# Performance work log

Hardware: AMD Instinct MI355X
Metric: run time of the kernel (lower is better)

Reference implementation:

```python
import jax, jax.numpy as jnp
import numpy as np

EPS = 1e-5


def _bn_relu(h, gamma, beta):
    # BatchNorm1d in training mode: stats over all but the last (channel) dim
    m = h.reshape(-1, h.shape[-1])
    mu = jnp.mean(m, axis=0)
    var = jnp.var(m, axis=0)
    return jax.nn.relu((h - mu) * jax.lax.rsqrt(var + EPS) * gamma + beta)


def setup_inputs() -> dict:
    key = jax.random.key(0)
    ks = jax.random.split(key, 16)
    B, N, D, OUT = 64, 64, 64, 128
    T = 2 * D          # object_tuple_size = 128
    HG, HF = 256, 128  # hidden_dim_g, hidden_dim_f

    def lin(k, i, o):
        return (jax.random.normal(k, (i, o), jnp.float32) / np.sqrt(i).astype(np.float32),
                jnp.zeros((o,), jnp.float32))

    inp = {"x": jax.random.normal(ks[0], (B, N, D), jnp.float32)}
    # G: depth-3 Linear-BN-ReLU, dims T -> HG -> HG -> T
    for i, (a, b) in enumerate([(T, HG), (HG, HG), (HG, T)]):
        W, bb = lin(ks[1 + i], a, b)
        inp[f"gW{i}"] = W
        inp[f"gb{i}"] = bb
        inp[f"gg{i}"] = jnp.ones((b,), jnp.float32)
        inp[f"gB{i}"] = jnp.zeros((b,), jnp.float32)
    # F: depth-2 Linear-BN-ReLU, dims T -> HF -> T, then Linear(T, OUT)
    for i, (a, b) in enumerate([(T, HF), (HF, T)]):
        W, bb = lin(ks[5 + i], a, b)
        inp[f"fW{i}"] = W
        inp[f"fb{i}"] = bb
        inp[f"fg{i}"] = jnp.ones((b,), jnp.float32)
        inp[f"fB{i}"] = jnp.zeros((b,), jnp.float32)
    inp["foW"], inp["fob"] = lin(ks[8], T, OUT)
    return inp


def reference(x, gW0, gb0, gg0, gB0, gW1, gb1, gg1, gB1, gW2, gb2, gg2, gB2,
              fW0, fb0, fg0, fB0, fW1, fb1, fg1, fB1, foW, fob):
    B, N, D = x.shape
    # GroupObjectsIntoPairs: all ordered pairs -> (B, N*N, 2D)
    xi = jnp.broadcast_to(x[:, :, None, :], (B, N, N, D))
    xj = jnp.broadcast_to(x[:, None, :, :], (B, N, N, D))
    h = jnp.concatenate([xi, xj], axis=-1).reshape(B, N * N, 2 * D)
    # G: per-pair MLP
    for W, b, g, be in ((gW0, gb0, gg0, gB0), (gW1, gb1, gg1, gB1), (gW2, gb2, gg2, gB2)):
        h = _bn_relu(h @ W + b, g, be)
    # sum over pair dimension (no layer norm)
    s = h.sum(axis=1)  # (B, 2D)
    # F: MLP + final linear
    for W, b, g, be in ((fW0, fb0, fg0, fB0), (fW1, fb1, fg1, fB1)):
        s = _bn_relu(s @ W + b, g, be)
    return s @ foW + fob  # (B, OUT)
```

## Files before the change

### kernel.cpp

```cpp
#include <hip/hip_runtime.h>


typedef _Float16 half8 __attribute__((ext_vector_type(8)));
typedef _Float16 half4_t __attribute__((ext_vector_type(4)));
typedef float float4_t __attribute__((ext_vector_type(4)));

static constexpr float kEps = 1e-5f;
static constexpr float kM = 262144.f;

static constexpr size_t OFF_U   = 0;
static constexpr size_t OFF_V   = OFF_U  + (size_t)4096*256*4;
static constexpr size_t OFF_UP  = OFF_V  + (size_t)4096*256*4;
static constexpr size_t OFF_VP  = OFF_UP + (size_t)4096*256*2;
static constexpr size_t OFF_W1T = OFF_VP + (size_t)4096*256*2;
static constexpr size_t OFF_W2T = OFF_W1T + (size_t)256*256*2;
static constexpr size_t OFF_Z1  = OFF_W2T + (size_t)128*256*2;
static constexpr size_t OFF_ST0 = OFF_Z1 + (size_t)262144*256*2;
static constexpr size_t OFF_C0S = OFF_ST0 + (size_t)64*4*256*4;
static constexpr size_t OFF_C0T = OFF_C0S + 1024;
static constexpr size_t OFF_C1S = OFF_C0T + 1024;
static constexpr size_t OFF_C1T = OFF_C1S + 1024;
static constexpr size_t OFF_C2S = OFF_C1T + 1024;
static constexpr size_t OFF_C2T = OFF_C2S + 512;
static constexpr size_t OFF_ST1 = OFF_C2T + 512;
static constexpr size_t OFF_ST2 = OFF_ST1 + (size_t)32*512*4;
static constexpr size_t OFF_SB  = OFF_ST2 + (size_t)32*256*4;
static constexpr size_t OFF_FST0 = OFF_SB + (size_t)64*128*4;
static constexpr size_t OFF_FST1 = OFF_FST0 + 1024;
static constexpr size_t ZERO_BYTES = (size_t)32*512*4 + (size_t)32*256*4
                                   + (size_t)64*128*4 + 2048;
static constexpr size_t OFF_FZ0  = OFF_FST1 + 1024;
static constexpr size_t OFF_FZ1  = OFF_FZ0 + (size_t)64*128*4;
static constexpr size_t OFF_CF0S = OFF_FZ1 + (size_t)64*128*4;
static constexpr size_t OFF_CF0T = OFF_CF0S + 512;
static constexpr size_t OFF_CF1S = OFF_CF0T + 512;
static constexpr size_t OFF_CF1T = OFF_CF1S + 512;
static constexpr size_t OFF_C1H  = OFF_CF1T + 512;
static constexpr size_t OFF_Z2   = OFF_C1H + 1024;
static constexpr size_t WS_REQUIRED = OFF_Z2 + (size_t)262144*128*2;

static __device__ inline half8 relu8(half8 s) {
#pragma unroll
  for (int e = 0; e < 8; ++e) s[e] = s[e] > (_Float16)0 ? s[e] : (_Float16)0;
  return s;
}

__global__ __launch_bounds__(256) void k_wt(const float* __restrict__ gW1,
                                            const float* __restrict__ gW2,
                                            _Float16* __restrict__ W1T,
                                            _Float16* __restrict__ W2T) {
  int idx = blockIdx.x * 256 + threadIdx.x;
  if (idx < 65536) {
    int n = idx >> 8, k = idx & 255;
    W1T[idx] = (_Float16)gW1[k * 256 + n];
  } else if (idx < 98304) {
    int j = idx - 65536;
    int n = j >> 8, k = j & 255;
    W2T[j] = (_Float16)gW2[k * 128 + n];
  }
}

__global__ __launch_bounds__(256) void k_prep(const float* __restrict__ x,
                                              const float* __restrict__ gW0,
                                              float* __restrict__ U,
                                              float* __restrict__ V) {
  __shared__ __align__(16) float sX[32 * 64];
  int t = threadIdx.x;
  int p0 = blockIdx.x * 32;
  int by = blockIdx.y;
  int hsel = by >> 1;
  int cbase = (by & 1) * 128;
#pragma unroll
  for (int it = 0; it < 2; ++it) {
    int f4 = (it * 256 + t) * 4;
    *(float4_t*)(sX + f4) = *(const float4_t*)(x + (size_t)p0 * 64 + f4);
  }
  __syncthreads();
  int r = t >> 3, cg = (t & 7) * 16;
  const float* Wb = gW0 + (size_t)(hsel * 64) * 256 + cbase + cg;
  float acc[16];
#pragma unroll
  for (int j = 0; j < 16; ++j) acc[j] = 0.f;
  for (int k = 0; k < 64; ++k) {
    float xv = sX[r * 64 + k];
    const float4_t* wr = (const float4_t*)(Wb + (size_t)k * 256);
    float4_t w0 = wr[0], w1 = wr[1], w2 = wr[2], w3 = wr[3];
#pragma unroll
    for (int j = 0; j < 4; ++j) {
      acc[j]      += xv * w0[j];
      acc[4 + j]  += xv * w1[j];
      acc[8 + j]  += xv * w2[j];
      acc[12 + j] += xv * w3[j];
    }
  }
  float* outp = (hsel ? V : U) + (size_t)(p0 + r) * 256 + cbase + cg;
#pragma unroll
  for (int q = 0; q < 4; ++q) {
    float4_t o = {acc[q * 4], acc[q * 4 + 1], acc[q * 4 + 2], acc[q * 4 + 3]};
    *(float4_t*)(outp + q * 4) = o;
  }
}

__global__ __launch_bounds__(256) void k_stats0(const float* __restrict__ U,
                                                const float* __restrict__ V,
                                                float* __restrict__ st0) {
  int b = blockIdx.x, c = threadIdx.x;
  float su = 0, su2 = 0, sv = 0, sv2 = 0;
  for (int i = 0; i < 64; ++i) {
    float u = U[(size_t)(b * 64 + i) * 256 + c];
    float v = V[(size_t)(b * 64 + i) * 256 + c];
    su += u; su2 += u * u; sv += v; sv2 += v * v;
  }
  st0[(b * 4 + 0) * 256 + c] = su;
  st0[(b * 4 + 1) * 256 + c] = su2;
  st0[(b * 4 + 2) * 256 + c] = sv;
  st0[(b * 4 + 3) * 256 + c] = sv2;
}

__global__ __launch_bounds__(256) void k_bn0(const float* __restrict__ st0,
                                             const float* __restrict__ gb0,
                                             const float* __restrict__ gg0,
                                             const float* __restrict__ gB0,
                                             float* __restrict__ c0s,
                                             float* __restrict__ c0t) {
  int c = threadIdx.x;
  float su = 0, su2 = 0, sv = 0, sv2 = 0, cross = 0;
  for (int b = 0; b < 64; ++b) {
    float a  = st0[(b * 4 + 0) * 256 + c];
    float a2 = st0[(b * 4 + 1) * 256 + c];
    float v  = st0[(b * 4 + 2) * 256 + c];
    float v2 = st0[(b * 4 + 3) * 256 + c];
    su += a; su2 += a2; sv += v; sv2 += v2; cross += a * v;
  }
  float b0 = gb0[c];
  float sumz  = 64.f * (su + sv) + kM * b0;
  float sumzz = 64.f * (su2 + sv2) + 2.f * cross + 2.f * b0 * 64.f * (su + sv) + kM * b0 * b0;
  float mu = sumz / kM;
  float var = sumzz / kM - mu * mu;
  float sc = gg0[c] * rsqrtf(var + kEps);
  c0s[c] = sc;
  c0t[c] = gB0[c] + sc * (b0 - mu);
}

__global__ __launch_bounds__(256) void k_uv(const float* __restrict__ U,
                                            const float* __restrict__ V,
                                            const float* __restrict__ c0s,
                                            const float* __restrict__ c0t,
                                            _Float16* __restrict__ Up,
                                            _Float16* __restrict__ Vp) {
  int idx = blockIdx.x * 256 + threadIdx.x;
  int e4 = idx * 4;
  int c4 = e4 & 255;
  float4_t u = *(const float4_t*)(U + e4);
  float4_t v = *(const float4_t*)(V + e4);
  float4_t s = *(const float4_t*)(c0s + c4);
  float4_t tt = *(const float4_t*)(c0t + c4);
  half4_t hu, hv;
#pragma unroll
  for (int e = 0; e < 4; ++e) {
    hu[e] = (_Float16)(u[e] * s[e] + tt[e]);
    hv[e] = (_Float16)(v[e] * s[e]);
  }
  *(half4_t*)(Up + e4) = hu;
  *(half4_t*)(Vp + e4) = hv;
}

__global__ __launch_bounds__(256) void k_gemm1(const _Float16* __restrict__ Up,
                                               const _Float16* __restrict__ Vp,
                                               const _Float16* __restrict__ W1T,
                                               const float* __restrict__ gb1,
                                               _Float16* __restrict__ Z1,
                                               float* __restrict__ stats1) {
  __shared__ __align__(16) _Float16 sU[2 * 264];
  __shared__ __align__(16) _Float16 sV[64 * 264];
  __shared__ __align__(16) _Float16 sW[128 * 72];
  const int t = threadIdx.x;
  const int bx = blockIdx.x;
  const int n0 = blockIdx.y * 128;
  const int b = bx >> 5;
  const int i0 = (bx & 31) * 2;
  const long R0 = (long)bx * 128;

  if (t < 64) {
    int row = t >> 5, k8 = (t & 31) * 8;
    *(half8*)(sU + row * 264 + k8) =
        *(const half8*)(Up + (size_t)(b * 64 + i0 + row) * 256 + k8);
  }
#pragma unroll
  for (int it = 0; it < 8; ++it) {
    int flat = it * 256 + t;
    int row = flat >> 5, k8 = (flat & 31) * 8;
    *(half8*)(sV + row * 264 + k8) =
        *(const half8*)(Vp + (size_t)(b * 64 + row) * 256 + k8);
  }

  const int wid = t >> 6, L = t & 63;
  const int wrow = wid >> 1, wcol = wid & 1;
  const int quad = L >> 4, l15 = L & 15;

  float4_t acc[4][4];
#pragma unroll
  for (int mt = 0; mt < 4; ++mt)
#pragma unroll
    for (int nt = 0; nt < 4; ++nt) acc[mt][nt] = (float4_t){0.f, 0.f, 0.f, 0.f};

  for (int kc = 0; kc < 4; ++kc) {
    __syncthreads();
#pragma unroll
    for (int it = 0; it < 4; ++it) {
      int flat = it * 256 + t;
      int n = flat >> 3, k8 = (flat & 7) * 8;
      *(half8*)(sW + n * 72 + k8) =
          *(const half8*)(W1T + (size_t)(n0 + n) * 256 + kc * 64 + k8);
    }
    __syncthreads();
#pragma unroll
    for (int ks = 0; ks < 2; ++ks) {
      const int kk = ks * 32 + quad * 8;
      const int kg = kc * 64 + kk;
      const half8 u = *(const half8*)(sU + wrow * 264 + kg);
      half8 afr[4];
#pragma unroll
      for (int mt = 0; mt < 4; ++mt) {
        half8 v = *(const half8*)(sV + (mt * 16 + l15) * 264 + kg);
        afr[mt] = relu8(u + v);
      }
      half8 bfr[4];
#pragma unroll
      for (int nt = 0; nt < 4; ++nt)
        bfr[nt] = *(const half8*)(sW + (wcol * 64 + nt * 16 + l15) * 72 + kk);
#pragma unroll
      for (int mt = 0; mt < 4; ++mt)
#pragma unroll
        for (int nt = 0; nt < 4; ++nt)
          acc[mt][nt] = __builtin_amdgcn_mfma_f32_16x16x32_f16(afr[mt], bfr[nt],
                                                               acc[mt][nt], 0, 0, 0);
    }
  }

  const int rep = bx & 31;
#pragma unroll
  for (int nt = 0; nt < 4; ++nt) {
    const int col = n0 + wcol * 64 + nt * 16 + l15;
    const float b1c = gb1[col];
    float sz = 0.f, szz = 0.f;
#pragma unroll
    for (int mt = 0; mt < 4; ++mt) {
      const size_t rowb = (size_t)(R0 + wrow * 64 + mt * 16 + quad * 4);
#pragma unroll
      for (int r = 0; r < 4; ++r) {
        float z = acc[mt][nt][r] + b1c;
        Z1[(rowb + r) * 256 + col] = (_Float16)z;
        sz += z;
        szz += z * z;
      }
    }
    sz += __shfl_xor(sz, 16, 64);
    sz += __shfl_xor(sz, 32, 64);
    szz += __shfl_xor(szz, 16, 64);
    szz += __shfl_xor(szz, 32, 64);
    if (quad == 0) {
      atomicAdd(stats1 + rep * 512 + col, sz);
      atomicAdd(stats1 + rep * 512 + 256 + col, szz);
    }
  }
}

__global__ __launch_bounds__(256) void k_bn1(const float* __restrict__ stats1,
                                             const float* __restrict__ gg1,
                                             const float* __restrict__ gB1,
                                             float* __restrict__ c1s,
                                             float* __restrict__ c1t,
                                             _Float16* __restrict__ c1h) {
  int c = threadIdx.x;
  float S = 0.f, S2 = 0.f;
  for (int rp = 0; rp < 32; ++rp) {
    S += stats1[rp * 512 + c];
    S2 += stats1[rp * 512 + 256 + c];
  }
  float mu = S / kM;
  float var = S2 / kM - mu * mu;
  float sc = gg1[c] * rsqrtf(var + kEps);
  float sh = gB1[c] - sc * mu;
  c1s[c] = sc;
  c1t[c] = sh;
  c1h[c] = (_Float16)sc;
  c1h[256 + c] = (_Float16)sh;
}

__global__ __launch_bounds__(256) void k_gemm2(const _Float16* __restrict__ Z1,
                                               const _Float16* __restrict__ W2T,
                                               const _Float16* __restrict__ c1h,
                                               const float* __restrict__ gb2,
                                               _Float16* __restrict__ Z2,
                                               float* __restrict__ stats2) {
  __shared__ __align__(16) _Float16 sA[128 * 72];
  __shared__ __align__(16) _Float16 sW[128 * 72];
  __shared__ __align__(16) _Float16 sSh[256];
  __shared__ __align__(16) _Float16 sTh[256];
  const int t = threadIdx.x;
  const int bx = blockIdx.x;
  const long R0 = (long)bx * 128;
  sSh[t] = c1h[t];
  sTh[t] = c1h[256 + t];

  const int wid = t >> 6, L = t & 63;
  const int wrow = wid >> 1, wcol = wid & 1;
  const int quad = L >> 4, l15 = L & 15;

  float4_t acc[4][4];
#pragma unroll
  for (int mt = 0; mt < 4; ++mt)
#pragma unroll
    for (int nt = 0; nt < 4; ++nt) acc[mt][nt] = (float4_t){0.f, 0.f, 0.f, 0.f};

  for (int kc = 0; kc < 4; ++kc) {
    __syncthreads();
#pragma unroll
    for (int it = 0; it < 4; ++it) {
      int flat = it * 256 + t;
      int row = flat >> 3, k8 = (flat & 7) * 8;
      int kg = kc * 64 + k8;
      half8 hv = *(const half8*)(Z1 + ((size_t)R0 + row) * 256 + kg);
      half8 hs = *(const half8*)(sSh + kg);
      half8 ht = *(const half8*)(sTh + kg);
      half8 ov = hv * hs + ht;
      ov = relu8(ov);
      *(half8*)(sA + row * 72 + k8) = ov;
    }
#pragma unroll
    for (int it = 0; it < 4; ++it) {
      int flat = it * 256 + t;
      int n = flat >> 3, k8 = (flat & 7) * 8;
      *(half8*)(sW + n * 72 + k8) =
          *(const half8*)(W2T + (size_t)n * 256 + kc * 64 + k8);
    }
    __syncthreads();
#pragma unroll
    for (int ks = 0; ks < 2; ++ks) {
      const int kk = ks * 32 + quad * 8;
      half8 afr[4];
#pragma unroll
      for (int mt = 0; mt < 4; ++mt)
        afr[mt] = *(const half8*)(sA + (wrow * 64 + mt * 16 + l15) * 72 + kk);
      half8 bfr[4];
#pragma unroll
      for (int nt = 0; nt < 4; ++nt)
        bfr[nt] = *(const half8*)(sW + (wcol * 64 + nt * 16 + l15) * 72 + kk);
#pragma unroll
      for (int mt = 0; mt < 4; ++mt)
#pragma unroll
        for (int nt = 0; nt < 4; ++nt)
          acc[mt][nt] = __builtin_amdgcn_mfma_f32_16x16x32_f16(afr[mt], bfr[nt],
                                                               acc[mt][nt], 0, 0, 0);
    }
  }

  const int rep = bx & 31;
#pragma unroll
  for (int nt = 0; nt < 4; ++nt) {
    const int col = wcol * 64 + nt * 16 + l15;
    const float b2c = gb2[col];
    float sz = 0.f, szz = 0.f;
#pragma unroll
    for (int mt = 0; mt < 4; ++mt) {
      const size_t rowb = (size_t)(R0 + wrow * 64 + mt * 16 + quad * 4);
#pragma unroll
      for (int r = 0; r < 4; ++r) {
        float z = acc[mt][nt][r] + b2c;
        Z2[(rowb + r) * 128 + col] = (_Float16)z;
        sz += z;
        szz += z * z;
      }
    }
    sz += __shfl_xor(sz, 16, 64);
    sz += __shfl_xor(sz, 32, 64);
    szz += __shfl_xor(szz, 16, 64);
    szz += __shfl_xor(szz, 32, 64);
    if (quad == 0) {
      atomicAdd(stats2 + rep * 256 + col, sz);
      atomicAdd(stats2 + rep * 256 + 128 + col, szz);
    }
  }
}

template <int FINAL>
__global__ __launch_bounds__(256) void k_gemm23(const _Float16* __restrict__ Z1,
                                                const _Float16* __restrict__ W2T,
                                                const float* __restrict__ c1s,
                                                const float* __restrict__ c1t,
                                                const float* __restrict__ gb2,
                                                const float* __restrict__ c2s,
                                                const float* __restrict__ c2t,
                                                float* __restrict__ stats2,
                                                float* __restrict__ sbuf) {
  __shared__ __align__(16) _Float16 sA[128 * 72];
  __shared__ __align__(16) _Float16 sW[128 * 72];
  __shared__ __align__(16) float sS[256];
  __shared__ __align__(16) float sT[256];
  const int t = threadIdx.x;
  const int bx = blockIdx.x;
  const long R0 = (long)bx * 128;
  sS[t] = c1s[t];
  sT[t] = c1t[t];

  const int wid = t >> 6, L = t & 63;
  const int wrow = wid >> 1, wcol = wid & 1;
  const int quad = L >> 4, l15 = L & 15;

  float4_t acc[4][4];
#pragma unroll
  for (int mt = 0; mt < 4; ++mt)
#pragma unroll
    for (int nt = 0; nt < 4; ++nt) acc[mt][nt] = (float4_t){0.f, 0.f, 0.f, 0.f};

  for (int kc = 0; kc < 4; ++kc) {
    __syncthreads();
#pragma unroll
    for (int it = 0; it < 4; ++it) {
      int flat = it * 256 + t;
      int row = flat >> 3, k8 = (flat & 7) * 8;
      int kg = kc * 64 + k8;
      half8 hv = *(const half8*)(Z1 + ((size_t)R0 + row) * 256 + kg);
      float4_t s0 = *(const float4_t*)(sS + kg);
      float4_t s1 = *(const float4_t*)(sS + kg + 4);
      float4_t t0 = *(const float4_t*)(sT + kg);
      float4_t t1 = *(const float4_t*)(sT + kg + 4);
      half8 ov;
#pragma unroll
      for (int e = 0; e < 4; ++e) {
        ov[e]     = (_Float16)fmaxf(s0[e] * (float)hv[e] + t0[e], 0.f);
        ov[4 + e] = (_Float16)fmaxf(s1[e] * (float)hv[4 + e] + t1[e], 0.f);
      }
      *(half8*)(sA + row * 72 + k8) = ov;
    }
#pragma unroll
    for (int it = 0; it < 4; ++it) {
      int flat = it * 256 + t;
      int n = flat >> 3, k8 = (flat & 7) * 8;
      *(half8*)(sW + n * 72 + k8) =
          *(const half8*)(W2T + (size_t)n * 256 + kc * 64 + k8);
    }
    __syncthreads();
#pragma unroll
    for (int ks = 0; ks < 2; ++ks) {
      const int kk = ks * 32 + quad * 8;
      half8 afr[4];
#pragma unroll
      for (int mt = 0; mt < 4; ++mt)
        afr[mt] = *(const half8*)(sA + (wrow * 64 + mt * 16 + l15) * 72 + kk);
      half8 bfr[4];
#pragma unroll
      for (int nt = 0; nt < 4; ++nt)
        bfr[nt] = *(const half8*)(sW + (wcol * 64 + nt * 16 + l15) * 72 + kk);
#pragma unroll
      for (int mt = 0; mt < 4; ++mt)
#pragma unroll
        for (int nt = 0; nt < 4; ++nt)
          acc[mt][nt] = __builtin_amdgcn_mfma_f32_16x16x32_f16(afr[mt], bfr[nt],
                                                               acc[mt][nt], 0, 0, 0);
    }
  }

  const int rep = bx & 31;
#pragma unroll
  for (int nt = 0; nt < 4; ++nt) {
    const int col = wcol * 64 + nt * 16 + l15;
    const float b2c = gb2[col];
    if (FINAL) {
      const float s2 = c2s[col], t2 = c2t[col];
      float ps = 0.f;
#pragma unroll
      for (int mt = 0; mt < 4; ++mt)
#pragma unroll
        for (int r = 0; r < 4; ++r)
          ps += fmaxf(s2 * (acc[mt][nt][r] + b2c) + t2, 0.f);
      ps += __shfl_xor(ps, 16, 64);
      ps += __shfl_xor(ps, 32, 64);
      if (quad == 0) atomicAdd(sbuf + (bx >> 5) * 128 + col, ps);
    } else {
      float sz = 0.f, szz = 0.f;
#pragma unroll
      for (int mt = 0; mt < 4; ++mt)
#pragma unroll
        for (int r = 0; r < 4; ++r) {
          float z = acc[mt][nt][r] + b2c;
          sz += z;
          szz += z * z;
        }
      sz += __shfl_xor(sz, 16, 64);
      sz += __shfl_xor(sz, 32, 64);
      szz += __shfl_xor(szz, 16, 64);
      szz += __shfl_xor(szz, 32, 64);
      if (quad == 0) {
        atomicAdd(stats2 + rep * 256 + col, sz);
        atomicAdd(stats2 + rep * 256 + 128 + col, szz);
      }
    }
  }
}

__global__ __launch_bounds__(128) void k_bn2(const float* __restrict__ stats2,
                                             const float* __restrict__ gg2,
                                             const float* __restrict__ gB2,
                                             float* __restrict__ c2s,
                                             float* __restrict__ c2t) {
  int c = threadIdx.x;
  float S = 0.f, S2 = 0.f;
  for (int rp = 0; rp < 32; ++rp) {
    S += stats2[rp * 256 + c];
    S2 += stats2[rp * 256 + 128 + c];
  }
  float mu = S / kM;
  float var = S2 / kM - mu * mu;
  float sc = gg2[c] * rsqrtf(var + kEps);
  c2s[c] = sc;
  c2t[c] = gB2[c] - sc * mu;
}

__global__ __launch_bounds__(256) void k_red(const _Float16* __restrict__ Z2,
                                             const float* __restrict__ c2s,
                                             const float* __restrict__ c2t,
                                             float* __restrict__ sbuf) {
  __shared__ float sR[256 * 8];
  const int t = threadIdx.x;
  const int bx = blockIdx.x;
  const int b = bx >> 5;
  const long row0 = (long)bx * 128;
  const int rr = t >> 4;
  const int c8 = (t & 15) * 8;

  float4_t s0 = *(const float4_t*)(c2s + c8);
  float4_t s1 = *(const float4_t*)(c2s + c8 + 4);
  float4_t t0 = *(const float4_t*)(c2t + c8);
  float4_t t1 = *(const float4_t*)(c2t + c8 + 4);

  float acc[8];
#pragma unroll
  for (int e = 0; e < 8; ++e) acc[e] = 0.f;
#pragma unroll
  for (int it = 0; it < 8; ++it) {
    long row = row0 + it * 16 + rr;
    half8 h = *(const half8*)(Z2 + row * 128 + c8);
#pragma unroll
    for (int e = 0; e < 4; ++e) {
      acc[e]     += fmaxf(s0[e] * (float)h[e] + t0[e], 0.f);
      acc[4 + e] += fmaxf(s1[e] * (float)h[4 + e] + t1[e], 0.f);
    }
  }
#pragma unroll
  for (int e = 0; e < 8; ++e) sR[t * 8 + e] = acc[e];
  __syncthreads();
  if (t < 128) {
    int g = t >> 3, e = t & 7;
    float S = 0.f;
#pragma unroll
    for (int rr2 = 0; rr2 < 16; ++rr2) S += sR[rr2 * 128 + t];
    (void)g; (void)e;
    atomicAdd(sbuf + b * 128 + t, S);
  }
}

template <bool APPLY_BN, bool STATS>
__global__ __launch_bounds__(256) void k_fg(const float* __restrict__ in,
                                            const float* __restrict__ cs,
                                            const float* __restrict__ ct,
                                            const float* __restrict__ W,
                                            const float* __restrict__ bias,
                                            float* __restrict__ zout,
                                            float* __restrict__ stats) {
  __shared__ __align__(16) float sIn[8 * 128];
  __shared__ __align__(16) float sZ[8 * 128];
  const int t = threadIdx.x;
  const int r0 = blockIdx.x * 8;
  {
    int flat = t * 4;
    int col = flat & 127;
    float4_t v = *(const float4_t*)(in + (size_t)r0 * 128 + flat);
    if (APPLY_BN) {
      float4_t s = *(const float4_t*)(cs + col);
      float4_t sh = *(const float4_t*)(ct + col);
#pragma unroll
      for (int e = 0; e < 4; ++e) v[e] = fmaxf(s[e] * v[e] + sh[e], 0.f);
    }
    *(float4_t*)(sIn + flat) = v;
  }
  __syncthreads();

  const int r = t >> 5;
  const int c4 = (t & 31) * 4;
  float4_t acc = *(const float4_t*)(bias + c4);
  for (int k = 0; k < 128; ++k) {
    float xv = sIn[r * 128 + k];
    float4_t w = *(const float4_t*)(W + (size_t)k * 128 + c4);
#pragma unroll
    for (int e = 0; e < 4; ++e) acc[e] += xv * w[e];
  }
  *(float4_t*)(zout + (size_t)(r0 + r) * 128 + c4) = acc;

  if (STATS) {
    *(float4_t*)(sZ + r * 128 + c4) = acc;
    __syncthreads();
    if (t < 128) {
      float S = 0.f, S2 = 0.f;
#pragma unroll
      for (int rr = 0; rr < 8; ++rr) {
        float z = sZ[rr * 128 + t];
        S += z;
        S2 += z * z;
      }
      atomicAdd(stats + t, S);
      atomicAdd(stats + 128 + t, S2);
    }
  }
}

__global__ __launch_bounds__(128) void k_fbn(const float* __restrict__ stats,
                                             const float* __restrict__ g,
                                             const float* __restrict__ B,
                                             float* __restrict__ cs,
                                             float* __restrict__ ct) {
  int c = threadIdx.x;
  float S = stats[c], S2 = stats[128 + c];
  float mu = S / 64.f;
  float var = S2 / 64.f - mu * mu;
  float sc = g[c] * rsqrtf(var + kEps);
  cs[c] = sc;
  ct[c] = B[c] - sc * mu;
}

extern "C" void kernel_launch(void* const* d_in, const int* in_sizes, int n_in,
                              void* d_out, int out_size, void* d_ws, size_t ws_size,
                              hipStream_t stream) {
  (void)in_sizes; (void)n_in; (void)out_size;
  const float* x   = (const float*)d_in[0];
  const float* gW0 = (const float*)d_in[1];
  const float* gb0 = (const float*)d_in[2];
  const float* gg0 = (const float*)d_in[3];
  const float* gB0 = (const float*)d_in[4];
  const float* gW1 = (const float*)d_in[5];
  const float* gb1 = (const float*)d_in[6];
  const float* gg1 = (const float*)d_in[7];
  const float* gB1 = (const float*)d_in[8];
  const float* gW2 = (const float*)d_in[9];
  const float* gb2 = (const float*)d_in[10];
  const float* gg2 = (const float*)d_in[11];
  const float* gB2 = (const float*)d_in[12];
  const float* fW0 = (const float*)d_in[13];
  const float* fb0 = (const float*)d_in[14];
  const float* fg0 = (const float*)d_in[15];
  const float* fB0 = (const float*)d_in[16];
  const float* fW1 = (const float*)d_in[17];
  const float* fb1 = (const float*)d_in[18];
  const float* fg1 = (const float*)d_in[19];
  const float* fB1 = (const float*)d_in[20];
  const float* foW = (const float*)d_in[21];
  const float* fob = (const float*)d_in[22];
  float* out = (float*)d_out;

  char* ws = (char*)d_ws;
  float*    U    = (float*)(ws + OFF_U);
  float*    V    = (float*)(ws + OFF_V);
  _Float16* Up   = (_Float16*)(ws + OFF_UP);
  _Float16* Vp   = (_Float16*)(ws + OFF_VP);
  _Float16* W1T  = (_Float16*)(ws + OFF_W1T);
  _Float16* W2T  = (_Float16*)(ws + OFF_W2T);
  _Float16* Z1   = (_Float16*)(ws + OFF_Z1);
  float*    st0  = (float*)(ws + OFF_ST0);
  float*    c0s  = (float*)(ws + OFF_C0S);
  float*    c0t  = (float*)(ws + OFF_C0T);
  float*    c1s  = (float*)(ws + OFF_C1S);
  float*    c1t  = (float*)(ws + OFF_C1T);
  float*    c2s  = (float*)(ws + OFF_C2S);
  float*    c2t  = (float*)(ws + OFF_C2T);
  float*    st1  = (float*)(ws + OFF_ST1);
  float*    st2  = (float*)(ws + OFF_ST2);
  float*    sbuf = (float*)(ws + OFF_SB);
  float*    fst0 = (float*)(ws + OFF_FST0);
  float*    fst1 = (float*)(ws + OFF_FST1);
  float*    fz0  = (float*)(ws + OFF_FZ0);
  float*    fz1  = (float*)(ws + OFF_FZ1);
  float*    cf0s = (float*)(ws + OFF_CF0S);
  float*    cf0t = (float*)(ws + OFF_CF0T);
  float*    cf1s = (float*)(ws + OFF_CF1S);
  float*    cf1t = (float*)(ws + OFF_CF1T);
  _Float16* c1h  = (_Float16*)(ws + OFF_C1H);
  _Float16* Z2   = (_Float16*)(ws + OFF_Z2);

  hipMemsetAsync(ws + OFF_ST1, 0, ZERO_BYTES, stream);

  k_wt<<<384, 256, 0, stream>>>(gW1, gW2, W1T, W2T);
  k_prep<<<dim3(128, 4), 256, 0, stream>>>(x, gW0, U, V);
  k_stats0<<<64, 256, 0, stream>>>(U, V, st0);
  k_bn0<<<1, 256, 0, stream>>>(st0, gb0, gg0, gB0, c0s, c0t);
  k_uv<<<1024, 256, 0, stream>>>(U, V, c0s, c0t, Up, Vp);
  k_gemm1<<<dim3(2048, 2), 256, 0, stream>>>(Up, Vp, W1T, gb1, Z1, st1);
  k_bn1<<<1, 256, 0, stream>>>(st1, gg1, gB1, c1s, c1t, c1h);

  if (ws_size >= WS_REQUIRED) {
    k_gemm2<<<2048, 256, 0, stream>>>(Z1, W2T, c1h, gb2, Z2, st2);
    k_bn2<<<1, 128, 0, stream>>>(st2, gg2, gB2, c2s, c2t);
    k_red<<<2048, 256, 0, stream>>>(Z2, c2s, c2t, sbuf);
  } else {
    k_gemm23<0><<<2048, 256, 0, stream>>>(Z1, W2T, c1s, c1t, gb2, c2s, c2t, st2, sbuf);
    k_bn2<<<1, 128, 0, stream>>>(st2, gg2, gB2, c2s, c2t);
    k_gemm23<1><<<2048, 256, 0, stream>>>(Z1, W2T, c1s, c1t, gb2, c2s, c2t, st2, sbuf);
  }

  k_fg<false, true><<<8, 256, 0, stream>>>(sbuf, nullptr, nullptr, fW0, fb0, fz0, fst0);
  k_fbn<<<1, 128, 0, stream>>>(fst0, fg0, fB0, cf0s, cf0t);
  k_fg<true, true><<<8, 256, 0, stream>>>(fz0, cf0s, cf0t, fW1, fb1, fz1, fst1);
  k_fbn<<<1, 128, 0, stream>>>(fst1, fg1, fB1, cf1s, cf1t);
  k_fg<true, false><<<8, 256, 0, stream>>>(fz1, cf1s, cf1t, foW, fob, out, nullptr);
}
```

Baseline: 322.1 us.

## Stage GEMM outputs through LDS for coalesced stores and shrink gemm1 shared memory

In k_gemm1 and k_gemm2 the MFMA accumulator results are now written into a padded LDS tile and then copied to global memory as 16-byte row-contiguous chunks. This replaces scattered 2-byte per-lane stores of Z1/Z2. k_gemm1 also loads U and V per K-chunk instead of preloading the full 256-wide rows, and reuses that buffer for output staging. This cuts LDS use from about 53KB to 35KB, which may raise occupancy. The cost is extra barriers and an LDS round trip in the epilogue.

```diff
diff --git a/kernel.cpp b/kernel.cpp
--- a/kernel.cpp
+++ b/kernel.cpp
@@ -171,9 +171,12 @@
                                                const float* __restrict__ gb1,
                                                _Float16* __restrict__ Z1,
                                                float* __restrict__ stats1) {
-  __shared__ __align__(16) _Float16 sU[2 * 264];
-  __shared__ __align__(16) _Float16 sV[64 * 264];
-  __shared__ __align__(16) _Float16 sW[128 * 72];
+  __shared__ __align__(16) char smem[128 * 136 * 2];
+  _Float16* sU = (_Float16*)smem;
+  _Float16* sV = (_Float16*)(smem + 288);
+  _Float16* sW = (_Float16*)(smem + 288 + 64 * 72 * 2);
+  _Float16* sO = (_Float16*)smem;
+
   const int t = threadIdx.x;
   const int bx = blockIdx.x;
   const int n0 = blockIdx.y * 128;
@@ -181,19 +184,6 @@
   const int i0 = (bx & 31) * 2;
   const long R0 = (long)bx * 128;
 
-  if (t < 64) {
-    int row = t >> 5, k8 = (t & 31) * 8;
-    *(half8*)(sU + row * 264 + k8) =
-        *(const half8*)(Up + (size_t)(b * 64 + i0 + row) * 256 + k8);
-  }
-#pragma unroll
-  for (int it = 0; it < 8; ++it) {
-    int flat = it * 256 + t;
-    int row = flat >> 5, k8 = (flat & 31) * 8;
-    *(half8*)(sV + row * 264 + k8) =
-        *(const half8*)(Vp + (size_t)(b * 64 + row) * 256 + k8);
-  }
-
   const int wid = t >> 6, L = t & 63;
   const int wrow = wid >> 1, wcol = wid & 1;
   const int quad = L >> 4, l15 = L & 15;
@@ -206,23 +196,34 @@
 
   for (int kc = 0; kc < 4; ++kc) {
     __syncthreads();
+    if (t < 16) {
+      int row = t >> 3, c8 = (t & 7) * 8;
+      *(half8*)(sU + row * 72 + c8) =
+          *(const half8*)(Up + (size_t)(b * 64 + i0 + row) * 256 + kc * 64 + c8);
+    }
+#pragma unroll
+    for (int it = 0; it < 2; ++it) {
+      int flat = it * 256 + t;
+      int row = flat >> 3, c8 = (flat & 7) * 8;
+      *(half8*)(sV + row * 72 + c8) =
+          *(const half8*)(Vp + (size_t)(b * 64 + row) * 256 + kc * 64 + c8);
+    }
 #pragma unroll
     for (int it = 0; it < 4; ++it) {
       int flat = it * 256 + t;
-      int n = flat >> 3, k8 = (flat & 7) * 8;
-      *(half8*)(sW + n * 72 + k8) =
-          *(const half8*)(W1T + (size_t)(n0 + n) * 256 + kc * 64 + k8);
+      int row = flat >> 3, c8 = (flat & 7) * 8;
+      *(half8*)(sW + row * 72 + c8) =
+          *(const half8*)(W1T + (size_t)(n0 + row) * 256 + kc * 64 + c8);
     }
     __syncthreads();
 #pragma unroll
     for (int ks = 0; ks < 2; ++ks) {
       const int kk = ks * 32 + quad * 8;
-      const int kg = kc * 64 + kk;
-      const half8 u = *(const half8*)(sU + wrow * 264 + kg);
+      const half8 u = *(const half8*)(sU + wrow * 72 + kk);
       half8 afr[4];
 #pragma unroll
       for (int mt = 0; mt < 4; ++mt) {
-        half8 v = *(const half8*)(sV + (mt * 16 + l15) * 264 + kg);
+        half8 v = *(const half8*)(sV + (mt * 16 + l15) * 72 + kk);
         afr[mt] = relu8(u + v);
       }
       half8 bfr[4];
@@ -238,19 +239,20 @@
     }
   }
 
+  __syncthreads();
   const int rep = bx & 31;
 #pragma unroll
   for (int nt = 0; nt < 4; ++nt) {
-    const int col = n0 + wcol * 64 + nt * 16 + l15;
-    const float b1c = gb1[col];
+    const int lcol = wcol * 64 + nt * 16 + l15;
+    const float b1c = gb1[n0 + lcol];
     float sz = 0.f, szz = 0.f;
 #pragma unroll
     for (int mt = 0; mt < 4; ++mt) {
-      const size_t rowb = (size_t)(R0 + wrow * 64 + mt * 16 + quad * 4);
+      const int lrow = wrow * 64 + mt * 16 + quad * 4;
 #pragma unroll
       for (int r = 0; r < 4; ++r) {
         float z = acc[mt][nt][r] + b1c;
-        Z1[(rowb + r) * 256 + col] = (_Float16)z;
+        sO[(lrow + r) * 136 + lcol] = (_Float16)z;
         sz += z;
         szz += z * z;
       }
@@ -260,9 +262,17 @@
     szz += __shfl_xor(szz, 16, 64);
     szz += __shfl_xor(szz, 32, 64);
     if (quad == 0) {
-      atomicAdd(stats1 + rep * 512 + col, sz);
-      atomicAdd(stats1 + rep * 512 + 256 + col, szz);
-    }
+      atomicAdd(stats1 + rep * 512 + n0 + lcol, sz);
+      atomicAdd(stats1 + rep * 512 + 256 + n0 + lcol, szz);
+    }
+  }
+  __syncthreads();
+#pragma unroll
+  for (int it = 0; it < 8; ++it) {
+    int cid = it * 256 + t;
+    int row = cid >> 4, ch = (cid & 15) * 8;
+    half8 hv = *(const half8*)(sO + row * 136 + ch);
+    *(half8*)(Z1 + (size_t)(R0 + row) * 256 + n0 + ch) = hv;
   }
 }
 
@@ -294,8 +304,10 @@
                                                const float* __restrict__ gb2,
                                                _Float16* __restrict__ Z2,
                                                float* __restrict__ stats2) {
-  __shared__ __align__(16) _Float16 sA[128 * 72];
-  __shared__ __align__(16) _Float16 sW[128 * 72];
+  __shared__ __align__(16) char smem[2 * 128 * 72 * 2];
+  _Float16* sA = (_Float16*)smem;
+  _Float16* sW = (_Float16*)(smem + 128 * 72 * 2);
+  _Float16* sO = (_Float16*)smem;
   __shared__ __align__(16) _Float16 sSh[256];
   __shared__ __align__(16) _Float16 sTh[256];
   const int t = threadIdx.x;
@@ -317,23 +329,26 @@
   for (int kc = 0; kc < 4; ++kc) {
     __syncthreads();
 #pragma unroll
-    for (int it = 0; it < 4; ++it) {
+    for (int it = 0; it < 2; ++it) {
       int flat = it * 256 + t;
       int row = flat >> 3, k8 = (flat & 7) * 8;
       int kg = kc * 64 + k8;
       half8 hv = *(const half8*)(Z1 + ((size_t)R0 + row) * 256 + kg);
       half8 hs = *(const half8*)(sSh + kg);
       half8 ht = *(const half8*)(sTh + kg);
-      half8 ov = hv * hs + ht;
-      ov = relu8(ov);
+      half8 ov = relu8(hv * hs + ht);
       *(half8*)(sA + row * 72 + k8) = ov;
+      int row2 = row + 64;
+      half8 hv2 = *(const half8*)(Z1 + ((size_t)R0 + row2) * 256 + kg);
+      half8 ov2 = relu8(hv2 * hs + ht);
+      *(half8*)(sA + row2 * 72 + k8) = ov2;
     }
 #pragma unroll
     for (int it = 0; it < 4; ++it) {
       int flat = it * 256 + t;
-      int n = flat >> 3, k8 = (flat & 7) * 8;
-      *(half8*)(sW + n * 72 + k8) =
-          *(const half8*)(W2T + (size_t)n * 256 + kc * 64 + k8);
+      int row = flat >> 3, k8 = (flat & 7) * 8;
+      *(half8*)(sW + row * 72 + k8) =
+          *(const half8*)(W2T + (size_t)row * 256 + kc * 64 + k8);
     }
     __syncthreads();
 #pragma unroll
@@ -356,19 +371,20 @@
     }
   }
 
+  __syncthreads();
   const int rep = bx & 31;
 #pragma unroll
   for (int nt = 0; nt < 4; ++nt) {
-    const int col = wcol * 64 + nt * 16 + l15;
-    const float b2c = gb2[col];
+    const int lcol = wcol * 64 + nt * 16 + l15;
+    const float b2c = gb2[lcol];
     float sz = 0.f, szz = 0.f;
 #pragma unroll
     for (int mt = 0; mt < 4; ++mt) {
-      const size_t rowb = (size_t)(R0 + wrow * 64 + mt * 16 + quad * 4);
+      const int lrow = wrow * 64 + mt * 16 + quad * 4;
 #pragma unroll
       for (int r = 0; r < 4; ++r) {
         float z = acc[mt][nt][r] + b2c;
-        Z2[(rowb + r) * 128 + col] = (_Float16)z;
+        sO[(lrow + r) * 136 + lcol] = (_Float16)z;
         sz += z;
         szz += z * z;
       }
@@ -378,9 +394,17 @@
     szz += __shfl_xor(szz, 16, 64);
     szz += __shfl_xor(szz, 32, 64);
     if (quad == 0) {
-      atomicAdd(stats2 + rep * 256 + col, sz);
-      atomicAdd(stats2 + rep * 256 + 128 + col, szz);
-    }
+      atomicAdd(stats2 + rep * 256 + lcol, sz);
+      atomicAdd(stats2 + rep * 256 + 128 + lcol, szz);
+    }
+  }
+  __syncthreads();
+#pragma unroll
+  for (int it = 0; it < 8; ++it) {
+    int cid = it * 256 + t;
+    int row = cid >> 4, ch = (cid & 15) * 8;
+    half8 hv = *(const half8*)(sO + row * 136 + ch);
+    *(half8*)(Z2 + (size_t)(R0 + row) * 128 + ch) = hv;
   }
 }
 
@@ -552,11 +576,9 @@
   for (int e = 0; e < 8; ++e) sR[t * 8 + e] = acc[e];
   __syncthreads();
   if (t < 128) {
-    int g = t >> 3, e = t & 7;
     float S = 0.f;
 #pragma unroll
     for (int rr2 = 0; rr2 < 16; ++rr2) S += sR[rr2 * 128 + t];
-    (void)g; (void)e;
     atomicAdd(sbuf + b * 128 + t, S);
   }
 }
```

Result: faster. 311.7 us (-3.2%).
